# Kernel optimization log

Hardware: AMD Instinct MI355X
Metric: run time of the kernel (lower is better)

The kernel has to match this reference:

```python
import jax, jax.numpy as jnp
import numpy as np

N_NODES = 100000
N_EDGES = 300000
HID = 256
N0, N1, N2 = 40000, 30000, 30000
D0, D1, D2 = 512, 256, 128


def setup_inputs() -> dict:
    key = jax.random.key(0)
    ks = jax.random.split(key, 14)
    s = 0.05  # init scale
    return {
        "feat0": jax.random.normal(ks[0], (N0, D0), jnp.float32),
        "feat1": jax.random.normal(ks[1], (N1, D1), jnp.float32),
        "feat2": jax.random.normal(ks[2], (N2, D2), jnp.float32),
        # per-type Linear(in_dim, HID) params (torch Linear: y = x @ W.T + b)
        "fc_w0": jax.random.normal(ks[3], (HID, D0), jnp.float32) * s,
        "fc_b0": jnp.zeros((HID,), jnp.float32),
        "fc_w1": jax.random.normal(ks[4], (HID, D1), jnp.float32) * s,
        "fc_b1": jnp.zeros((HID,), jnp.float32),
        "fc_w2": jax.random.normal(ks[5], (HID, D2), jnp.float32) * s,
        "fc_b2": jnp.zeros((HID,), jnp.float32),
        # GraphConv 1: weight=False, bias=True
        "gc1_bias": jnp.zeros((HID,), jnp.float32),
        # GraphConv 2: weight (in,out) + bias (DGL convention: feat @ W)
        "gc2_weight": jax.random.normal(ks[6], (HID, HID), jnp.float32) * s,
        "gc2_bias": jnp.zeros((HID,), jnp.float32),
        "semantic_weight": jax.random.normal(ks[7], (1, 5), jnp.float32),
        "src": jax.random.randint(ks[8], (N_EDGES,), 0, N_NODES, jnp.int64),
        "dst": jax.random.randint(ks[9], (N_EDGES,), 0, N_NODES, jnp.int64),
    }


def reference(feat0, feat1, feat2, fc_w0, fc_b0, fc_w1, fc_b1, fc_w2, fc_b2,
              gc1_bias, gc2_weight, gc2_bias, semantic_weight, src, dst):
    # per-type projection then concat along node dim -> [N_NODES, HID]
    h = jnp.concatenate([
        feat0 @ fc_w0.T + fc_b0,
        feat1 @ fc_w1.T + fc_b1,
        feat2 @ fc_w2.T + fc_b2,
    ], axis=0)

    ones = jnp.ones((src.shape[0],), h.dtype)
    deg_out = jnp.maximum(jax.ops.segment_sum(ones, src, num_segments=N_NODES), 1.0)
    deg_in = jnp.maximum(jax.ops.segment_sum(ones, dst, num_segments=N_NODES), 1.0)
    norm_out = jax.lax.rsqrt(deg_out)[:, None]  # D_out^{-1/2}
    norm_in = jax.lax.rsqrt(deg_in)[:, None]    # D_in^{-1/2}

    def gconv(x, W, b):
        # DGL GraphConv, norm='both': D_in^{-1/2} A D_out^{-1/2} x W + b, relu
        msg = (x * norm_out)[src]                                  # [E, HID]
        agg = jax.ops.segment_sum(msg, dst, num_segments=N_NODES)  # [N, HID]
        agg = agg * norm_in
        if W is not None:
            agg = agg @ W
        return jax.nn.relu(agg + b)

    # dropout is identity in eval mode
    h = gconv(h, None, gc1_bias)        # layer 0: weight=False
    h = gconv(h, gc2_weight, gc2_bias)  # layer 1
    return h, semantic_weight
```

## Files before the change

kernel.cpp:

```cpp
#include <hip/hip_runtime.h>
#include <cstdint>

#define HID 256
static constexpr int    NNODES = 100000;
static constexpr int    NEDGES = 300000;
static constexpr size_t NH     = (size_t)NNODES * HID;
static constexpr int    SCAN_B = 256;
static constexpr int    NSBLK  = (NNODES + SCAN_B - 1) / SCAN_B;

typedef __attribute__((ext_vector_type(8))) short bf16x8;
typedef __attribute__((ext_vector_type(4))) float f32x4;

__device__ __forceinline__ unsigned short f2bf(float x) {
    unsigned int u = __float_as_uint(x);
    u += 0x7fffu + ((u >> 16) & 1u);
    return (unsigned short)(u >> 16);
}
__device__ __forceinline__ unsigned int pack2(float a, float b) {
    return (unsigned int)f2bf(a) | ((unsigned int)f2bf(b) << 16);
}
__device__ __forceinline__ float bflo(unsigned int u) { return __uint_as_float(u << 16); }
__device__ __forceinline__ float bfhi(unsigned int u) { return __uint_as_float(u & 0xffff0000u); }

__global__ void zero_i32_k(int* __restrict__ p, int n) {
    int i = blockIdx.x * blockDim.x + threadIdx.x;
    if (i < n) p[i] = 0;
}

__global__ void count_deg_k(const int* __restrict__ src, const int* __restrict__ dst,
                            int* __restrict__ degout, int* __restrict__ degin) {
    int e = blockIdx.x * blockDim.x + threadIdx.x;
    if (e < NEDGES) {
        atomicAdd(degout + src[e], 1);
        atomicAdd(degin  + dst[e], 1);
    }
}

__global__ void cvt_weights_k(const float* __restrict__ w0, const float* __restrict__ w1,
                              const float* __restrict__ w2, const float* __restrict__ wg,
                              unsigned short* __restrict__ o0, unsigned short* __restrict__ o1,
                              unsigned short* __restrict__ o2, unsigned short* __restrict__ ogT) {
    int b = blockIdx.x, t = threadIdx.x;
    const float* in; unsigned short* out; int i;
    if (b < 128)      { in = w0; out = o0; i = b * 256 + t; }
    else if (b < 192) { in = w1; out = o1; i = (b - 128) * 256 + t; }
    else if (b < 224) { in = w2; out = o2; i = (b - 192) * 256 + t; }
    else {
        int n = b - 224, k = t;
        ogT[n * 256 + k] = f2bf(wg[k * 256 + n]);
        return;
    }
    float4 v = ((const float4*)in)[i];
    ushort4 w;
    w.x = f2bf(v.x); w.y = f2bf(v.y); w.z = f2bf(v.z); w.w = f2bf(v.w);
    ((ushort4*)out)[i] = w;
}

__global__ void scan_a_k(const int* __restrict__ degin, const int* __restrict__ degout,
                         int* __restrict__ row_off, int* __restrict__ bsums,
                         float* __restrict__ nout, float* __restrict__ nin,
                         const float* __restrict__ sw, float* __restrict__ tail) {
    __shared__ int sm[SCAN_B];
    int t = threadIdx.x;
    int g = blockIdx.x * SCAN_B + t;
    int v = (g < NNODES) ? degin[g] : 0;
    sm[t] = v;
    if (g < NNODES) {
        nout[g] = rsqrtf(fmaxf((float)degout[g], 1.0f));
        nin[g]  = rsqrtf(fmaxf((float)v, 1.0f));
    }
    if (g < 5) tail[g] = sw[g];
    __syncthreads();
#pragma unroll
    for (int off = 1; off < SCAN_B; off <<= 1) {
        int x = (t >= off) ? sm[t - off] : 0;
        __syncthreads();
        sm[t] += x;
        __syncthreads();
    }
    if (g < NNODES) row_off[g] = sm[t] - v;
    if (t == SCAN_B - 1) bsums[blockIdx.x] = sm[t];
}

__global__ void scan_b_k(int* __restrict__ bsums) {
    __shared__ int sm[512];
    int t = threadIdx.x;
    int v = (t < NSBLK) ? bsums[t] : 0;
    sm[t] = v;
    __syncthreads();
#pragma unroll
    for (int off = 1; off < 512; off <<= 1) {
        int x = (t >= off) ? sm[t - off] : 0;
        __syncthreads();
        sm[t] += x;
        __syncthreads();
    }
    if (t < NSBLK) bsums[t] = sm[t] - v;
}

__global__ void scan_c_k(int* __restrict__ row_off, const int* __restrict__ bsums) {
    int g = blockIdx.x * SCAN_B + threadIdx.x;
    if (g < NNODES) row_off[g] += bsums[blockIdx.x];
    if (g == 0) row_off[NNODES] = NEDGES;
}

__global__ void fill_csr_k(const int* __restrict__ src, const int* __restrict__ dst,
                           const int* __restrict__ row_off, int* __restrict__ cursor,
                           int* __restrict__ csr_src) {
    int e = blockIdx.x * blockDim.x + threadIdx.x;
    if (e < NEDGES) {
        int d = dst[e];
        int pos = row_off[d] + atomicAdd(cursor + d, 1);
        csr_src[pos] = src[e];
    }
}

template <int EPI>
__global__ __launch_bounds__(256) void gather_k(
    const unsigned short* __restrict__ h, const int* __restrict__ row_off,
    const int* __restrict__ csr_src, const float* __restrict__ nin,
    const float* __restrict__ bias, void* __restrict__ outv)
{
    int node = blockIdx.x * 4 + (threadIdx.x >> 6);
    if (node >= NNODES) return;
    int lane = threadIdx.x & 63;
    int beg = row_off[node], end = row_off[node + 1];
    float a0 = 0.f, a1 = 0.f, a2 = 0.f, a3 = 0.f;
    for (int base = beg; base < end; base += 64) {
        int cnt = end - base; if (cnt > 64) cnt = 64;
        int idx = csr_src[base + (lane < cnt ? lane : cnt - 1)];
        int j = 0;
        for (; j + 4 <= cnt; j += 4) {
            int s0 = __shfl(idx, j);
            int s1 = __shfl(idx, j + 1);
            int s2 = __shfl(idx, j + 2);
            int s3 = __shfl(idx, j + 3);
            uint2 v0 = *(const uint2*)(h + (size_t)s0 * HID + lane * 4);
            uint2 v1 = *(const uint2*)(h + (size_t)s1 * HID + lane * 4);
            uint2 v2 = *(const uint2*)(h + (size_t)s2 * HID + lane * 4);
            uint2 v3 = *(const uint2*)(h + (size_t)s3 * HID + lane * 4);
            a0 += bflo(v0.x) + bflo(v1.x) + bflo(v2.x) + bflo(v3.x);
            a1 += bfhi(v0.x) + bfhi(v1.x) + bfhi(v2.x) + bfhi(v3.x);
            a2 += bflo(v0.y) + bflo(v1.y) + bflo(v2.y) + bflo(v3.y);
            a3 += bfhi(v0.y) + bfhi(v1.y) + bfhi(v2.y) + bfhi(v3.y);
        }
        for (; j < cnt; ++j) {
            int s = __shfl(idx, j);
            uint2 v = *(const uint2*)(h + (size_t)s * HID + lane * 4);
            a0 += bflo(v.x); a1 += bfhi(v.x);
            a2 += bflo(v.y); a3 += bfhi(v.y);
        }
    }
    if (EPI) {
        float ni = nin[node];
        float4 bb = *(const float4*)(bias + lane * 4);
        float4 o;
        o.x = fmaxf(fmaf(a0, ni, bb.x), 0.f);
        o.y = fmaxf(fmaf(a1, ni, bb.y), 0.f);
        o.z = fmaxf(fmaf(a2, ni, bb.z), 0.f);
        o.w = fmaxf(fmaf(a3, ni, bb.w), 0.f);
        *(float4*)((float*)outv + (size_t)node * HID + lane * 4) = o;
    } else {
        ushort4 o;
        o.x = f2bf(a0); o.y = f2bf(a1); o.z = f2bf(a2); o.w = f2bf(a3);
        *(ushort4*)((unsigned short*)outv + (size_t)node * HID + lane * 4) = o;
    }
}

__global__ __launch_bounds__(256, 3) void proj_mfma_k(
    const float* __restrict__ f0, const float* __restrict__ f1, const float* __restrict__ f2,
    const unsigned short* __restrict__ w0, const unsigned short* __restrict__ w1,
    const unsigned short* __restrict__ w2,
    const float* __restrict__ b0, const float* __restrict__ b1, const float* __restrict__ b2,
    const float* __restrict__ nout, unsigned short* __restrict__ h0)
{
    __shared__ unsigned short As[64 * 32];
    __shared__ unsigned short Bs[256 * 32];

    int bx = blockIdx.x;
    const float* A; const unsigned short* B; const float* bias; const float* rs;
    unsigned short* C; int M, K;
    if (bx < 625)       { A = f0; B = w0; bias = b0; rs = nout;          C = h0;                          M = 40000; K = 512; }
    else if (bx < 1094) { bx -= 625;  A = f1; B = w1; bias = b1; rs = nout + 40000; C = h0 + (size_t)40000 * HID; M = 30000; K = 256; }
    else                { bx -= 1094; A = f2; B = w2; bias = b2; rs = nout + 70000; C = h0 + (size_t)70000 * HID; M = 30000; K = 128; }
    const int m0 = bx * 64;

    const int tid  = threadIdx.x;
    const int wn   = tid >> 6;
    const int lane = tid & 63;
    const int half = lane >> 4;
    const int l15  = lane & 15;

    f32x4 acc[4][4];
#pragma unroll
    for (int i = 0; i < 4; ++i)
#pragma unroll
        for (int j = 0; j < 4; ++j)
#pragma unroll
            for (int r = 0; r < 4; ++r) acc[i][j][r] = 0.f;

    const int arow = tid >> 2, ac = tid & 3;
    const int aslot = ac ^ ((arow >> 1) & 3);
    int agm = m0 + arow; if (agm > M - 1) agm = M - 1;

    for (int k0 = 0; k0 < K; k0 += 32) {
        {
            const float* p = A + (size_t)agm * K + k0 + ac * 8;
            float4 v0 = *(const float4*)p;
            float4 v1 = *(const float4*)(p + 4);
            uint4 u;
            u.x = pack2(v0.x, v0.y); u.y = pack2(v0.z, v0.w);
            u.z = pack2(v1.x, v1.y); u.w = pack2(v1.z, v1.w);
            *(uint4*)&As[(arow * 4 + aslot) * 8] = u;
        }
#pragma unroll
        for (int t = 0; t < 4; ++t) {
            int q = tid + t * 256;
            int row = q >> 2, c = q & 3;
            int slot = c ^ ((row >> 1) & 3);
            uint4 v = *(const uint4*)(B + (size_t)row * K + k0 + c * 8);
            *(uint4*)&Bs[(row * 4 + slot) * 8] = v;
        }
        __syncthreads();

        bf16x8 af[4], bfr[4];
#pragma unroll
        for (int i = 0; i < 4; ++i) {
            int m = i * 16 + l15;
            int ca = half ^ ((m >> 1) & 3);
            af[i] = *(const bf16x8*)&As[(m * 4 + ca) * 8];
            int n = wn * 64 + i * 16 + l15;
            int cb = half ^ ((n >> 1) & 3);
            bfr[i] = *(const bf16x8*)&Bs[(n * 4 + cb) * 8];
        }
#pragma unroll
        for (int i = 0; i < 4; ++i)
#pragma unroll
            for (int j = 0; j < 4; ++j)
                acc[i][j] = __builtin_amdgcn_mfma_f32_16x16x32_bf16(
                    af[i], bfr[j], acc[i][j], 0, 0, 0);
        __syncthreads();
    }

    float bj[4];
#pragma unroll
    for (int j = 0; j < 4; ++j) bj[j] = bias[wn * 64 + j * 16 + l15];
#pragma unroll
    for (int i = 0; i < 4; ++i)
#pragma unroll
        for (int r = 0; r < 4; ++r) {
            int m = m0 + i * 16 + (lane >> 4) * 4 + r;
            if (m >= M) continue;
            float rsm = rs[m];
#pragma unroll
            for (int j = 0; j < 4; ++j) {
                int n = wn * 64 + j * 16 + l15;
                C[(size_t)m * HID + n] = f2bf((acc[i][j][r] + bj[j]) * rsm);
            }
        }
}

__global__ __launch_bounds__(256, 3) void mid_mfma_k(
    const unsigned short* __restrict__ agg1, const unsigned short* __restrict__ wT,
    const float* __restrict__ b1, const float* __restrict__ nin,
    const float* __restrict__ nout, unsigned short* __restrict__ h2)
{
    __shared__ unsigned short As[64 * 32];
    __shared__ unsigned short Bs[256 * 32];

    const int m0   = blockIdx.x * 64;
    const int tid  = threadIdx.x;
    const int wn   = tid >> 6;
    const int lane = tid & 63;
    const int half = lane >> 4;
    const int l15  = lane & 15;

    f32x4 acc[4][4];
#pragma unroll
    for (int i = 0; i < 4; ++i)
#pragma unroll
        for (int j = 0; j < 4; ++j)
#pragma unroll
            for (int r = 0; r < 4; ++r) acc[i][j][r] = 0.f;

    const int arow = tid >> 2, ac = tid & 3;
    const int aslot = ac ^ ((arow >> 1) & 3);
    int agm = m0 + arow; if (agm > NNODES - 1) agm = NNODES - 1;
    const float ni = nin[agm], no = nout[agm];

    for (int k0 = 0; k0 < 256; k0 += 32) {
        {
            uint4 u = *(const uint4*)(agg1 + (size_t)agm * HID + k0 + ac * 8);
            float4 c0 = *(const float4*)(b1 + k0 + ac * 8);
            float4 c1 = *(const float4*)(b1 + k0 + ac * 8 + 4);
            float x0 = fmaxf(fmaf(bflo(u.x), ni, c0.x), 0.f) * no;
            float x1 = fmaxf(fmaf(bfhi(u.x), ni, c0.y), 0.f) * no;
            float x2 = fmaxf(fmaf(bflo(u.y), ni, c0.z), 0.f) * no;
            float x3 = fmaxf(fmaf(bfhi(u.y), ni, c0.w), 0.f) * no;
            float x4 = fmaxf(fmaf(bflo(u.z), ni, c1.x), 0.f) * no;
            float x5 = fmaxf(fmaf(bfhi(u.z), ni, c1.y), 0.f) * no;
            float x6 = fmaxf(fmaf(bflo(u.w), ni, c1.z), 0.f) * no;
            float x7 = fmaxf(fmaf(bfhi(u.w), ni, c1.w), 0.f) * no;
            uint4 o;
            o.x = pack2(x0, x1); o.y = pack2(x2, x3);
            o.z = pack2(x4, x5); o.w = pack2(x6, x7);
            *(uint4*)&As[(arow * 4 + aslot) * 8] = o;
        }
#pragma unroll
        for (int t = 0; t < 4; ++t) {
            int q = tid + t * 256;
            int row = q >> 2, c = q & 3;
            int slot = c ^ ((row >> 1) & 3);
            uint4 v = *(const uint4*)(wT + (size_t)row * 256 + k0 + c * 8);
            *(uint4*)&Bs[(row * 4 + slot) * 8] = v;
        }
        __syncthreads();

        bf16x8 af[4], bfr[4];
#pragma unroll
        for (int i = 0; i < 4; ++i) {
            int m = i * 16 + l15;
            int ca = half ^ ((m >> 1) & 3);
            af[i] = *(const bf16x8*)&As[(m * 4 + ca) * 8];
            int n = wn * 64 + i * 16 + l15;
            int cb = half ^ ((n >> 1) & 3);
            bfr[i] = *(const bf16x8*)&Bs[(n * 4 + cb) * 8];
        }
#pragma unroll
        for (int i = 0; i < 4; ++i)
#pragma unroll
            for (int j = 0; j < 4; ++j)
                acc[i][j] = __builtin_amdgcn_mfma_f32_16x16x32_bf16(
                    af[i], bfr[j], acc[i][j], 0, 0, 0);
        __syncthreads();
    }

#pragma unroll
    for (int i = 0; i < 4; ++i)
#pragma unroll
        for (int r = 0; r < 4; ++r) {
            int m = m0 + i * 16 + (lane >> 4) * 4 + r;
            if (m >= NNODES) continue;
#pragma unroll
            for (int j = 0; j < 4; ++j) {
                int n = wn * 64 + j * 16 + l15;
                h2[(size_t)m * HID + n] = f2bf(acc[i][j][r]);
            }
        }
}

extern "C" void kernel_launch(void* const* d_in, const int* in_sizes, int n_in,
                              void* d_out, int out_size, void* d_ws, size_t ws_size,
                              hipStream_t stream)
{
    const float* feat0    = (const float*)d_in[0];
    const float* feat1    = (const float*)d_in[1];
    const float* feat2    = (const float*)d_in[2];
    const float* fc_w0    = (const float*)d_in[3];
    const float* fc_b0    = (const float*)d_in[4];
    const float* fc_w1    = (const float*)d_in[5];
    const float* fc_b1    = (const float*)d_in[6];
    const float* fc_w2    = (const float*)d_in[7];
    const float* fc_b2    = (const float*)d_in[8];
    const float* gc1_bias = (const float*)d_in[9];
    const float* gc2_w    = (const float*)d_in[10];
    const float* gc2_bias = (const float*)d_in[11];
    const float* sw       = (const float*)d_in[12];
    const int*   src      = (const int*)d_in[13];
    const int*   dst      = (const int*)d_in[14];

    unsigned short* h0b  = (unsigned short*)d_ws;
    unsigned short* agg1 = h0b + NH;
    unsigned short* h2b  = h0b;
    unsigned short* w0b  = agg1 + NH;
    unsigned short* w1b  = w0b + 131072;
    unsigned short* w2b  = w1b + 65536;
    unsigned short* w2Tb = w2b + 32768;
    float* nout = (float*)(w2Tb + 65536);
    float* nin  = nout + NNODES;
    int* deg_out = (int*)(nin + NNODES);
    int* deg_in  = deg_out + NNODES;
    int* cursor  = deg_in + NNODES;
    int* row_off = cursor + NNODES;
    int* bsums   = row_off + NNODES + 1;
    int* csr_src = bsums + 512;
    float* out   = (float*)d_out;

    zero_i32_k<<<(3 * NNODES + 255) / 256, 256, 0, stream>>>(deg_out, 3 * NNODES);
    cvt_weights_k<<<480, 256, 0, stream>>>(fc_w0, fc_w1, fc_w2, gc2_w,
                                           w0b, w1b, w2b, w2Tb);
    count_deg_k<<<(NEDGES + 255) / 256, 256, 0, stream>>>(src, dst, deg_out, deg_in);
    scan_a_k<<<NSBLK, SCAN_B, 0, stream>>>(deg_in, deg_out, row_off, bsums,
                                           nout, nin, sw, out + NH);
    scan_b_k<<<1, 512, 0, stream>>>(bsums);
    scan_c_k<<<NSBLK, SCAN_B, 0, stream>>>(row_off, bsums);
    fill_csr_k<<<(NEDGES + 255) / 256, 256, 0, stream>>>(src, dst, row_off, cursor, csr_src);

    proj_mfma_k<<<1563, 256, 0, stream>>>(feat0, feat1, feat2, w0b, w1b, w2b,
                                          fc_b0, fc_b1, fc_b2, nout, h0b);

    gather_k<0><<<(NNODES + 3) / 4, 256, 0, stream>>>(h0b, row_off, csr_src,
                                                      nullptr, nullptr, agg1);

    mid_mfma_k<<<(NNODES + 63) / 64, 256, 0, stream>>>(agg1, w2Tb, gc1_bias,
                                                       nin, nout, h2b);

    gather_k<1><<<(NNODES + 3) / 4, 256, 0, stream>>>(h2b, row_off, csr_src,
                                                      nin, gc2_bias, out);
}
```

Before: 402.5 us.

## Load GEMM B fragments directly to registers and double-buffer A tile

```diff
diff --git a/kernel.cpp b/kernel.cpp
--- a/kernel.cpp
+++ b/kernel.cpp
@@ -174,8 +174,7 @@
     const float* __restrict__ b0, const float* __restrict__ b1, const float* __restrict__ b2,
     const float* __restrict__ nout, unsigned short* __restrict__ h0)
 {
-    __shared__ unsigned short As[64 * 32];
-    __shared__ unsigned short Bs[256 * 32];
+    __shared__ unsigned short As[2][64 * 32];
 
     int bx = blockIdx.x;
     const float* A; const unsigned short* B; const float* bias; const float* rs;
@@ -202,44 +201,57 @@
     const int arow = tid >> 2, ac = tid & 3;
     const int aslot = ac ^ ((arow >> 1) & 3);
     int agm = m0 + arow; if (agm > M - 1) agm = M - 1;
-
-    for (int k0 = 0; k0 < K; k0 += 32) {
+    const float* ap = A + (size_t)agm * K + ac * 8;
+
+    const unsigned short* bp = B + (size_t)(wn * 64 + l15) * K + half * 8;
+
+    const int nT = K >> 5;
+
+    float4 a0 = *(const float4*)ap;
+    float4 a1 = *(const float4*)(ap + 4);
+    bf16x8 bcur[4];
+#pragma unroll
+    for (int j = 0; j < 4; ++j) bcur[j] = *(const bf16x8*)(bp + (size_t)j * 16 * K);
+
+    for (int t = 0; t < nT; ++t) {
+        const int p = t & 1;
         {
-            const float* p = A + (size_t)agm * K + k0 + ac * 8;
-            float4 v0 = *(const float4*)p;
-            float4 v1 = *(const float4*)(p + 4);
             uint4 u;
-            u.x = pack2(v0.x, v0.y); u.y = pack2(v0.z, v0.w);
-            u.z = pack2(v1.x, v1.y); u.w = pack2(v1.z, v1.w);
-            *(uint4*)&As[(arow * 4 + aslot) * 8] = u;
-        }
-#pragma unroll
-        for (int t = 0; t < 4; ++t) {
-            int q = tid + t * 256;
-            int row = q >> 2, c = q & 3;
-            int slot = c ^ ((row >> 1) & 3);
-            uint4 v = *(const uint4*)(B + (size_t)row * K + k0 + c * 8);
-            *(uint4*)&Bs[(row * 4 + slot) * 8] = v;
-        }
-        __syncthreads();
-
-        bf16x8 af[4], bfr[4];
+            u.x = pack2(a0.x, a0.y); u.y = pack2(a0.z, a0.w);
+            u.z = pack2(a1.x, a1.y); u.w = pack2(a1.z, a1.w);
+            *(uint4*)&As[p][(arow * 4 + aslot) * 8] = u;
+        }
+        asm volatile("s_waitcnt lgkmcnt(0)" ::: "memory");
+        __builtin_amdgcn_s_barrier();
+        asm volatile("" ::: "memory");
+        __builtin_amdgcn_sched_barrier(0);
+
+        const int tn = (t + 1 < nT) ? t + 1 : t;
+        {
+            const float* pn = ap + tn * 32;
+            a0 = *(const float4*)pn;
+            a1 = *(const float4*)(pn + 4);
+        }
+        bf16x8 bnext[4];
+#pragma unroll
+        for (int j = 0; j < 4; ++j)
+            bnext[j] = *(const bf16x8*)(bp + (size_t)j * 16 * K + tn * 32);
+
+        bf16x8 af[4];
 #pragma unroll
         for (int i = 0; i < 4; ++i) {
             int m = i * 16 + l15;
             int ca = half ^ ((m >> 1) & 3);
-            af[i] = *(const bf16x8*)&As[(m * 4 + ca) * 8];
-            int n = wn * 64 + i * 16 + l15;
-            int cb = half ^ ((n >> 1) & 3);
-            bfr[i] = *(const bf16x8*)&Bs[(n * 4 + cb) * 8];
+            af[i] = *(const bf16x8*)&As[p][(m * 4 + ca) * 8];
         }
 #pragma unroll
         for (int i = 0; i < 4; ++i)
 #pragma unroll
             for (int j = 0; j < 4; ++j)
                 acc[i][j] = __builtin_amdgcn_mfma_f32_16x16x32_bf16(
-                    af[i], bfr[j], acc[i][j], 0, 0, 0);
-        __syncthreads();
+                    af[i], bcur[j], acc[i][j], 0, 0, 0);
+#pragma unroll
+        for (int j = 0; j < 4; ++j) bcur[j] = bnext[j];
     }
 
     float bj[4];
@@ -265,8 +277,7 @@
     const float* __restrict__ b1, const float* __restrict__ nin,
     const float* __restrict__ nout, unsigned short* __restrict__ h2)
 {
-    __shared__ unsigned short As[64 * 32];
-    __shared__ unsigned short Bs[256 * 32];
+    __shared__ unsigned short As[2][64 * 32];
 
     const int m0   = blockIdx.x * 64;
     const int tid  = threadIdx.x;
@@ -287,52 +298,61 @@
     const int aslot = ac ^ ((arow >> 1) & 3);
     int agm = m0 + arow; if (agm > NNODES - 1) agm = NNODES - 1;
     const float ni = nin[agm], no = nout[agm];
-
-    for (int k0 = 0; k0 < 256; k0 += 32) {
+    const unsigned short* ap = agg1 + (size_t)agm * HID + ac * 8;
+    const unsigned short* bp = wT + (size_t)(wn * 64 + l15) * 256 + half * 8;
+
+    uint4 au = *(const uint4*)ap;
+    bf16x8 bcur[4];
+#pragma unroll
+    for (int j = 0; j < 4; ++j) bcur[j] = *(const bf16x8*)(bp + (size_t)j * 16 * 256);
+
+#pragma unroll 2
+    for (int t = 0; t < 8; ++t) {
+        const int p = t & 1;
         {
-            uint4 u = *(const uint4*)(agg1 + (size_t)agm * HID + k0 + ac * 8);
+            const int k0 = t * 32;
             float4 c0 = *(const float4*)(b1 + k0 + ac * 8);
             float4 c1 = *(const float4*)(b1 + k0 + ac * 8 + 4);
-            float x0 = fmaxf(fmaf(bflo(u.x), ni, c0.x), 0.f) * no;
-            float x1 = fmaxf(fmaf(bfhi(u.x), ni, c0.y), 0.f) * no;
-            float x2 = fmaxf(fmaf(bflo(u.y), ni, c0.z), 0.f) * no;
-            float x3 = fmaxf(fmaf(bfhi(u.y), ni, c0.w), 0.f) * no;
-            float x4 = fmaxf(fmaf(bflo(u.z), ni, c1.x), 0.f) * no;
-            float x5 = fmaxf(fmaf(bfhi(u.z), ni, c1.y), 0.f) * no;
-            float x6 = fmaxf(fmaf(bflo(u.w), ni, c1.z), 0.f) * no;
-            float x7 = fmaxf(fmaf(bfhi(u.w), ni, c1.w), 0.f) * no;
+            float x0 = fmaxf(fmaf(bflo(au.x), ni, c0.x), 0.f) * no;
+            float x1 = fmaxf(fmaf(bfhi(au.x), ni, c0.y), 0.f) * no;
+            float x2 = fmaxf(fmaf(bflo(au.y), ni, c0.z), 0.f) * no;
+            float x3 = fmaxf(fmaf(bfhi(au.y), ni, c0.w), 0.f) * no;
+            float x4 = fmaxf(fmaf(bflo(au.z), ni, c1.x), 0.f) * no;
+            float x5 = fmaxf(fmaf(bfhi(au.z), ni, c1.y), 0.f) * no;
+            float x6 = fmaxf(fmaf(bflo(au.w), ni, c1.z), 0.f) * no;
+            float x7 = fmaxf(fmaf(bfhi(au.w), ni, c1.w), 0.f) * no;
             uint4 o;
             o.x = pack2(x0, x1); o.y = pack2(x2, x3);
             o.z = pack2(x4, x5); o.w = pack2(x6, x7);
-            *(uint4*)&As[(arow * 4 + aslot) * 8] = o;
-        }
-#pragma unroll
-        for (int t = 0; t < 4; ++t) {
-            int q = tid + t * 256;
-            int row = q >> 2, c = q & 3;
-            int slot = c ^ ((row >> 1) & 3);
-            uint4 v = *(const uint4*)(wT + (size_t)row * 256 + k0 + c * 8);
-            *(uint4*)&Bs[(row * 4 + slot) * 8] = v;
-        }
-        __syncthreads();
-
-        bf16x8 af[4], bfr[4];
+            *(uint4*)&As[p][(arow * 4 + aslot) * 8] = o;
+        }
+        asm volatile("s_waitcnt lgkmcnt(0)" ::: "memory");
+        __builtin_amdgcn_s_barrier();
+        asm volatile("" ::: "memory");
+        __builtin_amdgcn_sched_barrier(0);
+
+        const int tn = (t + 1 < 8) ? t + 1 : t;
+        au = *(const uint4*)(ap + tn * 32);
+        bf16x8 bnext[4];
+#pragma unroll
+        for (int j = 0; j < 4; ++j)
+            bnext[j] = *(const bf16x8*)(bp + (size_t)j * 16 * 256 + tn * 32);
+
+        bf16x8 af[4];
 #pragma unroll
         for (int i = 0; i < 4; ++i) {
             int m = i * 16 + l15;
             int ca = half ^ ((m >> 1) & 3);
-            af[i] = *(const bf16x8*)&As[(m * 4 + ca) * 8];
-            int n = wn * 64 + i * 16 + l15;
-            int cb = half ^ ((n >> 1) & 3);
-            bfr[i] = *(const bf16x8*)&Bs[(n * 4 + cb) * 8];
+            af[i] = *(const bf16x8*)&As[p][(m * 4 + ca) * 8];
         }
 #pragma unroll
         for (int i = 0; i < 4; ++i)
 #pragma unroll
             for (int j = 0; j < 4; ++j)
                 acc[i][j] = __builtin_amdgcn_mfma_f32_16x16x32_bf16(
-                    af[i], bfr[j], acc[i][j], 0, 0, 0);
-        __syncthreads();
+                    af[i], bcur[j], acc[i][j], 0, 0, 0);
+#pragma unroll
+        for (int j = 0; j < 4; ++j) bcur[j] = bnext[j];
     }
 
 #pragma unroll
```

Result: no change. 402.8 us (+0.1%).

## Restructure projection and mid GEMMs with 128-row tiles and register-prefetched pipeline

Applied to the files above, without the earlier changes.

```diff
diff --git a/kernel.cpp b/kernel.cpp
--- a/kernel.cpp
+++ b/kernel.cpp
@@ -167,26 +167,27 @@
     }
 }
 
-__global__ __launch_bounds__(256, 3) void proj_mfma_k(
+__global__ __launch_bounds__(512, 4) void proj_mfma_k(
     const float* __restrict__ f0, const float* __restrict__ f1, const float* __restrict__ f2,
     const unsigned short* __restrict__ w0, const unsigned short* __restrict__ w1,
     const unsigned short* __restrict__ w2,
     const float* __restrict__ b0, const float* __restrict__ b1, const float* __restrict__ b2,
     const float* __restrict__ nout, unsigned short* __restrict__ h0)
 {
-    __shared__ unsigned short As[64 * 32];
-    __shared__ unsigned short Bs[256 * 32];
+    __shared__ unsigned short As[2][128 * 32];
 
     int bx = blockIdx.x;
     const float* A; const unsigned short* B; const float* bias; const float* rs;
     unsigned short* C; int M, K;
-    if (bx < 625)       { A = f0; B = w0; bias = b0; rs = nout;          C = h0;                          M = 40000; K = 512; }
-    else if (bx < 1094) { bx -= 625;  A = f1; B = w1; bias = b1; rs = nout + 40000; C = h0 + (size_t)40000 * HID; M = 30000; K = 256; }
-    else                { bx -= 1094; A = f2; B = w2; bias = b2; rs = nout + 70000; C = h0 + (size_t)70000 * HID; M = 30000; K = 128; }
-    const int m0 = bx * 64;
+    if (bx < 313)       { A = f0; B = w0; bias = b0; rs = nout;          C = h0;                          M = 40000; K = 512; }
+    else if (bx < 548)  { bx -= 313; A = f1; B = w1; bias = b1; rs = nout + 40000; C = h0 + (size_t)40000 * HID; M = 30000; K = 256; }
+    else                { bx -= 548; A = f2; B = w2; bias = b2; rs = nout + 70000; C = h0 + (size_t)70000 * HID; M = 30000; K = 128; }
+    const int m0 = bx * 128;
 
     const int tid  = threadIdx.x;
-    const int wn   = tid >> 6;
+    const int wid  = tid >> 6;
+    const int wm   = wid >> 2;
+    const int wn   = wid & 3;
     const int lane = tid & 63;
     const int half = lane >> 4;
     const int l15  = lane & 15;
@@ -202,75 +203,88 @@
     const int arow = tid >> 2, ac = tid & 3;
     const int aslot = ac ^ ((arow >> 1) & 3);
     int agm = m0 + arow; if (agm > M - 1) agm = M - 1;
-
-    for (int k0 = 0; k0 < K; k0 += 32) {
-        {
-            const float* p = A + (size_t)agm * K + k0 + ac * 8;
-            float4 v0 = *(const float4*)p;
-            float4 v1 = *(const float4*)(p + 4);
-            uint4 u;
-            u.x = pack2(v0.x, v0.y); u.y = pack2(v0.z, v0.w);
-            u.z = pack2(v1.x, v1.y); u.w = pack2(v1.z, v1.w);
-            *(uint4*)&As[(arow * 4 + aslot) * 8] = u;
+    const float* ap = A + (size_t)agm * K + ac * 8;
+
+    const unsigned short* bp = B + (size_t)(wn * 64 + l15 * 4) * K + half * 8;
+
+    const int nT = K >> 5;
+
+    float4 a0E = *(const float4*)ap;
+    float4 a1E = *(const float4*)(ap + 4);
+    float4 a0O = *(const float4*)(ap + 32);
+    float4 a1O = *(const float4*)(ap + 36);
+    bf16x8 bcur[4];
+
+#define PROJ_STEP(P, A0, A1)                                                   \
+    {                                                                          \
+        uint4 u;                                                               \
+        u.x = pack2(A0.x, A0.y); u.y = pack2(A0.z, A0.w);                      \
+        u.z = pack2(A1.x, A1.y); u.w = pack2(A1.z, A1.w);                      \
+        *(uint4*)&As[P][(arow * 4 + aslot) * 8] = u;                           \
+        _Pragma("unroll")                                                      \
+        for (int j = 0; j < 4; ++j)                                            \
+            bcur[j] = *(const bf16x8*)(bp + (size_t)j * K + (tt + P) * 32);    \
+        asm volatile("s_waitcnt lgkmcnt(0)" ::: "memory");                     \
+        __builtin_amdgcn_s_barrier();                                          \
+        __builtin_amdgcn_sched_barrier(0);                                     \
+        {                                                                      \
+            int tf = tt + P + 2; if (tf > nT - 1) tf = nT - 1;                 \
+            const float* pn = ap + tf * 32;                                    \
+            A0 = *(const float4*)pn; A1 = *(const float4*)(pn + 4);            \
+        }                                                                      \
+        bf16x8 af[4];                                                          \
+        _Pragma("unroll")                                                      \
+        for (int i = 0; i < 4; ++i) {                                          \
+            int m = wm * 64 + i * 16 + l15;                                    \
+            int ca = half ^ ((m >> 1) & 3);                                    \
+            af[i] = *(const bf16x8*)&As[P][(m * 4 + ca) * 8];                  \
+        }                                                                      \
+        _Pragma("unroll")                                                      \
+        for (int i = 0; i < 4; ++i)                                            \
+            _Pragma("unroll")                                                  \
+            for (int j = 0; j < 4; ++j)                                        \
+                acc[i][j] = __builtin_amdgcn_mfma_f32_16x16x32_bf16(           \
+                    af[i], bcur[j], acc[i][j], 0, 0, 0);                       \
+    }
+
+    for (int tt = 0; tt < nT; tt += 2) {
+        PROJ_STEP(0, a0E, a1E)
+        PROJ_STEP(1, a0O, a1O)
+    }
+#undef PROJ_STEP
+
+    float4 bb = *(const float4*)(bias + wn * 64 + l15 * 4);
+    const int mwb = m0 + wm * 64;
+#pragma unroll
+    for (int i = 0; i < 4; ++i) {
+        int mb = mwb + i * 16 + half * 4;
+        if (mb >= M) continue;
+        float4 rv = *(const float4*)(rs + mb);
+#pragma unroll
+        for (int r = 0; r < 4; ++r) {
+            float rsm = (&rv.x)[r];
+            ushort4 o;
+            o.x = f2bf((acc[i][0][r] + bb.x) * rsm);
+            o.y = f2bf((acc[i][1][r] + bb.y) * rsm);
+            o.z = f2bf((acc[i][2][r] + bb.z) * rsm);
+            o.w = f2bf((acc[i][3][r] + bb.w) * rsm);
+            *(ushort4*)&C[(size_t)(mb + r) * HID + wn * 64 + l15 * 4] = o;
         }
-#pragma unroll
-        for (int t = 0; t < 4; ++t) {
-            int q = tid + t * 256;
-            int row = q >> 2, c = q & 3;
-            int slot = c ^ ((row >> 1) & 3);
-            uint4 v = *(const uint4*)(B + (size_t)row * K + k0 + c * 8);
-            *(uint4*)&Bs[(row * 4 + slot) * 8] = v;
-        }
-        __syncthreads();
-
-        bf16x8 af[4], bfr[4];
-#pragma unroll
-        for (int i = 0; i < 4; ++i) {
-            int m = i * 16 + l15;
-            int ca = half ^ ((m >> 1) & 3);
-            af[i] = *(const bf16x8*)&As[(m * 4 + ca) * 8];
-            int n = wn * 64 + i * 16 + l15;
-            int cb = half ^ ((n >> 1) & 3);
-            bfr[i] = *(const bf16x8*)&Bs[(n * 4 + cb) * 8];
-        }
-#pragma unroll
-        for (int i = 0; i < 4; ++i)
-#pragma unroll
-            for (int j = 0; j < 4; ++j)
-                acc[i][j] = __builtin_amdgcn_mfma_f32_16x16x32_bf16(
-                    af[i], bfr[j], acc[i][j], 0, 0, 0);
-        __syncthreads();
-    }
-
-    float bj[4];
-#pragma unroll
-    for (int j = 0; j < 4; ++j) bj[j] = bias[wn * 64 + j * 16 + l15];
-#pragma unroll
-    for (int i = 0; i < 4; ++i)
-#pragma unroll
-        for (int r = 0; r < 4; ++r) {
-            int m = m0 + i * 16 + (lane >> 4) * 4 + r;
-            if (m >= M) continue;
-            float rsm = rs[m];
-#pragma unroll
-            for (int j = 0; j < 4; ++j) {
-                int n = wn * 64 + j * 16 + l15;
-                C[(size_t)m * HID + n] = f2bf((acc[i][j][r] + bj[j]) * rsm);
-            }
-        }
-}
-
-__global__ __launch_bounds__(256, 3) void mid_mfma_k(
+    }
+}
+
+__global__ __launch_bounds__(512, 4) void mid_mfma_k(
     const unsigned short* __restrict__ agg1, const unsigned short* __restrict__ wT,
     const float* __restrict__ b1, const float* __restrict__ nin,
     const float* __restrict__ nout, unsigned short* __restrict__ h2)
 {
-    __shared__ unsigned short As[64 * 32];
-    __shared__ unsigned short Bs[256 * 32];
-
-    const int m0   = blockIdx.x * 64;
+    __shared__ unsigned short As[2][128 * 32];
+
+    const int m0   = blockIdx.x * 128;
     const int tid  = threadIdx.x;
-    const int wn   = tid >> 6;
+    const int wid  = tid >> 6;
+    const int wm   = wid >> 2;
+    const int wn   = wid & 3;
     const int lane = tid & 63;
     const int half = lane >> 4;
     const int l15  = lane & 15;
@@ -287,66 +301,79 @@
     const int aslot = ac ^ ((arow >> 1) & 3);
     int agm = m0 + arow; if (agm > NNODES - 1) agm = NNODES - 1;
     const float ni = nin[agm], no = nout[agm];
-
-    for (int k0 = 0; k0 < 256; k0 += 32) {
-        {
-            uint4 u = *(const uint4*)(agg1 + (size_t)agm * HID + k0 + ac * 8);
-            float4 c0 = *(const float4*)(b1 + k0 + ac * 8);
-            float4 c1 = *(const float4*)(b1 + k0 + ac * 8 + 4);
-            float x0 = fmaxf(fmaf(bflo(u.x), ni, c0.x), 0.f) * no;
-            float x1 = fmaxf(fmaf(bfhi(u.x), ni, c0.y), 0.f) * no;
-            float x2 = fmaxf(fmaf(bflo(u.y), ni, c0.z), 0.f) * no;
-            float x3 = fmaxf(fmaf(bfhi(u.y), ni, c0.w), 0.f) * no;
-            float x4 = fmaxf(fmaf(bflo(u.z), ni, c1.x), 0.f) * no;
-            float x5 = fmaxf(fmaf(bfhi(u.z), ni, c1.y), 0.f) * no;
-            float x6 = fmaxf(fmaf(bflo(u.w), ni, c1.z), 0.f) * no;
-            float x7 = fmaxf(fmaf(bfhi(u.w), ni, c1.w), 0.f) * no;
-            uint4 o;
-            o.x = pack2(x0, x1); o.y = pack2(x2, x3);
-            o.z = pack2(x4, x5); o.w = pack2(x6, x7);
-            *(uint4*)&As[(arow * 4 + aslot) * 8] = o;
+    const unsigned short* ap = agg1 + (size_t)agm * HID + ac * 8;
+    const unsigned short* bp = wT + (size_t)(wn * 64 + l15 * 4) * 256 + half * 8;
+
+    uint4  auE = *(const uint4*)ap;
+    uint4  auO = *(const uint4*)(ap + 32);
+    float4 cE0 = *(const float4*)(b1 + ac * 8);
+    float4 cE1 = *(const float4*)(b1 + ac * 8 + 4);
+    float4 cO0 = *(const float4*)(b1 + 32 + ac * 8);
+    float4 cO1 = *(const float4*)(b1 + 32 + ac * 8 + 4);
+    bf16x8 bcur[4];
+
+#define MID_STEP(P, AU, C0, C1)                                                \
+    {                                                                          \
+        float x0 = fmaxf(fmaf(bflo(AU.x), ni, C0.x), 0.f) * no;                \
+        float x1 = fmaxf(fmaf(bfhi(AU.x), ni, C0.y), 0.f) * no;                \
+        float x2 = fmaxf(fmaf(bflo(AU.y), ni, C0.z), 0.f) * no;                \
+        float x3 = fmaxf(fmaf(bfhi(AU.y), ni, C0.w), 0.f) * no;                \
+        float x4 = fmaxf(fmaf(bflo(AU.z), ni, C1.x), 0.f) * no;                \
+        float x5 = fmaxf(fmaf(bfhi(AU.z), ni, C1.y), 0.f) * no;                \
+        float x6 = fmaxf(fmaf(bflo(AU.w), ni, C1.z), 0.f) * no;                \
+        float x7 = fmaxf(fmaf(bfhi(AU.w), ni, C1.w), 0.f) * no;                \
+        uint4 o;                                                               \
+        o.x = pack2(x0, x1); o.y = pack2(x2, x3);                              \
+        o.z = pack2(x4, x5); o.w = pack2(x6, x7);                              \
+        *(uint4*)&As[P][(arow * 4 + aslot) * 8] = o;                           \
+        _Pragma("unroll")                                                      \
+        for (int j = 0; j < 4; ++j)                                            \
+            bcur[j] = *(const bf16x8*)(bp + j * 256 + (tt + P) * 32);          \
+        asm volatile("s_waitcnt lgkmcnt(0)" ::: "memory");                     \
+        __builtin_amdgcn_s_barrier();                                          \
+        __builtin_amdgcn_sched_barrier(0);                                     \
+        {                                                                      \
+            int tf = tt + P + 2; if (tf > 7) tf = 7;                           \
+            AU = *(const uint4*)(ap + tf * 32);                                \
+            C0 = *(const float4*)(b1 + tf * 32 + ac * 8);                      \
+            C1 = *(const float4*)(b1 + tf * 32 + ac * 8 + 4);                  \
+        }                                                                      \
+        bf16x8 af[4];                                                          \
+        _Pragma("unroll")                                                      \
+        for (int i = 0; i < 4; ++i) {                                          \
+            int m = wm * 64 + i * 16 + l15;                                    \
+            int ca = half ^ ((m >> 1) & 3);                                    \
+            af[i] = *(const bf16x8*)&As[P][(m * 4 + ca) * 8];                  \
+        }                                                                      \
+        _Pragma("unroll")                                                      \
+        for (int i = 0; i < 4; ++i)                                            \
+            _Pragma("unroll")                                                  \
+            for (int j = 0; j < 4; ++j)                                        \
+                acc[i][j] = __builtin_amdgcn_mfma_f32_16x16x32_bf16(           \
+                    af[i], bcur[j], acc[i][j], 0, 0, 0);                       \
+    }
+
+    for (int tt = 0; tt < 8; tt += 2) {
+        MID_STEP(0, auE, cE0, cE1)
+        MID_STEP(1, auO, cO0, cO1)
+    }
+#undef MID_STEP
+
+    const int mwb = m0 + wm * 64;
+#pragma unroll
+    for (int i = 0; i < 4; ++i) {
+        int mb = mwb + i * 16 + half * 4;
+        if (mb >= NNODES) continue;
+#pragma unroll
+        for (int r = 0; r < 4; ++r) {
+            ushort4 o;
+            o.x = f2bf(acc[i][0][r]);
+            o.y = f2bf(acc[i][1][r]);
+            o.z = f2bf(acc[i][2][r]);
+            o.w = f2bf(acc[i][3][r]);
+            *(ushort4*)&h2[(size_t)(mb + r) * HID + wn * 64 + l15 * 4] = o;
         }
-#pragma unroll
-        for (int t = 0; t < 4; ++t) {
-            int q = tid + t * 256;
-            int row = q >> 2, c = q & 3;
-            int slot = c ^ ((row >> 1) & 3);
-            uint4 v = *(const uint4*)(wT + (size_t)row * 256 + k0 + c * 8);
-            *(uint4*)&Bs[(row * 4 + slot) * 8] = v;
-        }
-        __syncthreads();
-
-        bf16x8 af[4], bfr[4];
-#pragma unroll
-        for (int i = 0; i < 4; ++i) {
-            int m = i * 16 + l15;
-            int ca = half ^ ((m >> 1) & 3);
-            af[i] = *(const bf16x8*)&As[(m * 4 + ca) * 8];
-            int n = wn * 64 + i * 16 + l15;
-            int cb = half ^ ((n >> 1) & 3);
-            bfr[i] = *(const bf16x8*)&Bs[(n * 4 + cb) * 8];
-        }
-#pragma unroll
-        for (int i = 0; i < 4; ++i)
-#pragma unroll
-            for (int j = 0; j < 4; ++j)
-                acc[i][j] = __builtin_amdgcn_mfma_f32_16x16x32_bf16(
-                    af[i], bfr[j], acc[i][j], 0, 0, 0);
-        __syncthreads();
-    }
-
-#pragma unroll
-    for (int i = 0; i < 4; ++i)
-#pragma unroll
-        for (int r = 0; r < 4; ++r) {
-            int m = m0 + i * 16 + (lane >> 4) * 4 + r;
-            if (m >= NNODES) continue;
-#pragma unroll
-            for (int j = 0; j < 4; ++j) {
-                int n = wn * 64 + j * 16 + l15;
-                h2[(size_t)m * HID + n] = f2bf(acc[i][j][r]);
-            }
-        }
+    }
 }
 
 extern "C" void kernel_launch(void* const* d_in, const int* in_sizes, int n_in,
@@ -396,14 +423,13 @@
     scan_c_k<<<NSBLK, SCAN_B, 0, stream>>>(row_off, bsums);
     fill_csr_k<<<(NEDGES + 255) / 256, 256, 0, stream>>>(src, dst, row_off, cursor, csr_src);
 
-    proj_mfma_k<<<1563, 256, 0, stream>>>(feat0, feat1, feat2, w0b, w1b, w2b,
-                                          fc_b0, fc_b1, fc_b2, nout, h0b);
+    proj_mfma_k<<<783, 512, 0, stream>>>(feat0, feat1, feat2, w0b, w1b, w2b,
+                                         fc_b0, fc_b1, fc_b2, nout, h0b);
 
     gather_k<0><<<(NNODES + 3) / 4, 256, 0, stream>>>(h0b, row_off, csr_src,
                                                       nullptr, nullptr, agg1);
 
-    mid_mfma_k<<<(NNODES + 63) / 64, 256, 0, stream>>>(agg1, w2Tb, gc1_bias,
-                                                       nin, nout, h2b);
+    mid_mfma_k<<<782, 512, 0, stream>>>(agg1, w2Tb, gc1_bias, nin, nout, h2b);
 
     gather_k<1><<<(NNODES + 3) / 4, 256, 0, stream>>>(h2b, row_off, csr_src,
                                                       nin, gc2_bias, out);
```

Result: slower. 441.6 us (+9.7%).
